# Kernel tuning notes

Measured on AMD Instinct MI355X. Metric: run time of the kernel, lower is better.

Reference implementation:

```python
import jax, jax.numpy as jnp
import numpy as np

EPS = 1e-8
SOFTEN = 1.0
COLOR_NORM = 1.0


def setup_inputs() -> dict:
    key = jax.random.key(0)
    k1, k2, k3, k4 = jax.random.split(key, 4)
    B, C, H, W = 16, 3, 224, 224
    K, HID = 64, 256
    img = jax.random.uniform(k1, (B, C, H, W), dtype=jnp.float32)
    W1 = jax.random.normal(k2, (HID, C), dtype=jnp.float32) * 0.1
    b1 = jax.random.normal(k3, (HID,), dtype=jnp.float32) * 0.1
    W2 = jax.random.normal(k4, (K, HID), dtype=jnp.float32) * 0.1
    return {"img": img, "W1": W1, "b1": b1, "W2": W2}


def reference(img, W1, b1, W2):
    # color_mask: 1x1 conv (3->256) + ReLU + 1x1 conv (256->K, no bias)
    h = jax.nn.relu(jnp.einsum('bchw,oc->bohw', img, W1) + b1[None, :, None, None])
    logits = jnp.einsum('bohw,ko->bkhw', h, W2)
    # Softmax2d == softmax over channel dim; soften=1
    m = jax.nn.softmax(SOFTEN * logits, axis=1)  # (B,K,H,W)
    # training=True path: soft weighted palette.
    # (img[:,:,None]*m[:,None]).sum(spatial) contracted directly via einsum
    # to avoid materializing the (B,3,K,H,W) broadcast tensor.
    num = jnp.einsum('bchw,bkhw->bck', img, m)          # (B,3,K)
    den = jnp.sum(m, axis=(2, 3))                        # (B,K)
    palette = num / (den[:, None, :] + EPS) / COLOR_NORM  # (B,3,K)
    # color_jitter=0 -> jitter_palette == palette
    transformed_img = jnp.einsum('bkhw,bck->bchw', m, palette)
    # match torch shape (B,3,K,1,1) for palette output
    return transformed_img, m, palette[:, :, :, None, None]
```

## Files before the change

kernel.cpp:

```cpp
#include <hip/hip_runtime.h>
#include <hip/hip_bf16.h>

#define BATCH 16
#define HW 50176
#define HID 256
#define K 64

#define OUT_T_OFF 0
#define OUT_M_OFF 2408448
#define OUT_P_OFF 53788672

#define WS_DEN 0
#define WS_NUM 1024
#define WS_W1P 4096
#define WS_W2B 5120

typedef short bf16x8 __attribute__((ext_vector_type(8)));
typedef float f32x4  __attribute__((ext_vector_type(4)));

static __device__ __forceinline__ short f2bf(float x) {
    union { __hip_bfloat16 h; short s; } u;
    u.h = __float2bfloat16(x);
    return u.s;
}

__global__ __launch_bounds__(256) void colorcnn_prep(
    const float* __restrict__ W1, const float* __restrict__ b1,
    const float* __restrict__ W2, float* __restrict__ wsf,
    float4* __restrict__ w1p, ushort* __restrict__ w2b)
{
    const int t = threadIdx.x;
    if (blockIdx.x == 0) {
#pragma unroll
        for (int q = 0; q < 16; ++q) wsf[q * 256 + t] = 0.f;
        w1p[t] = make_float4(W1[3 * t], W1[3 * t + 1], W1[3 * t + 2], b1[t]);
    }
#pragma unroll
    for (int q = 0; q < 8; ++q) {
        const int i = (blockIdx.x * 8 + q) * 256 + t;
        w2b[i] = (ushort)f2bf(W2[i]);
    }
}

__global__ __launch_bounds__(256) void colorcnn_mlp_softmax(
    const float* __restrict__ img, const float4* __restrict__ w1p,
    const ushort* __restrict__ w2b, float* __restrict__ m_out,
    float* __restrict__ den_ws, float* __restrict__ num_ws)
{
    __shared__ int4 lds[2304];
    __shared__ float sred[4][256];

    const int t = threadIdx.x;
    const int4* w2b16 = (const int4*)w2b;
#pragma unroll
    for (int q = 0; q < 8; ++q) {
        const int i = t + q * 256;
        const int n = i >> 5, s = i & 31;
        lds[n * 32 + (s ^ (n & 7))] = w2b16[i];
    }
    lds[2048 + (t ^ ((t >> 3) & 3))] = ((const int4*)w1p)[t];
    __syncthreads();

    const int b    = blockIdx.y;
    const int pb   = blockIdx.x * 256;
    const int w    = t >> 6;
    const int lane = t & 63;
    const int l15  = lane & 15;
    const int lg   = lane >> 4;
    const int pwb  = pb + w * 64;

    const float* ip = img + (size_t)b * 3 * HW;

    float rr[4], gg[4], uu[4];
#pragma unroll
    for (int s = 0; s < 4; ++s) {
        const int px = pwb + s * 16 + l15;
        rr[s] = ip[px]; gg[s] = ip[HW + px]; uu[s] = ip[2 * HW + px];
    }

    f32x4 acc[4][4];
#pragma unroll
    for (int s = 0; s < 4; ++s)
#pragma unroll
        for (int ni = 0; ni < 4; ++ni)
            acc[s][ni] = (f32x4){0.f, 0.f, 0.f, 0.f};

#pragma unroll
    for (int c = 0; c < 8; ++c) {
        bf16x8 a0, a1, a2, a3;
#pragma unroll
        for (int j = 0; j < 8; ++j) {
            const int hid = c * 32 + lg * 8 + j;
            const float4 wv = *(const float4*)&lds[2048 + (hid ^ lg)];
            float t0 = fmaf(rr[0], wv.x, fmaf(gg[0], wv.y, fmaf(uu[0], wv.z, wv.w)));
            float t1 = fmaf(rr[1], wv.x, fmaf(gg[1], wv.y, fmaf(uu[1], wv.z, wv.w)));
            float t2 = fmaf(rr[2], wv.x, fmaf(gg[2], wv.y, fmaf(uu[2], wv.z, wv.w)));
            float t3 = fmaf(rr[3], wv.x, fmaf(gg[3], wv.y, fmaf(uu[3], wv.z, wv.w)));
            a0[j] = f2bf(fmaxf(t0, 0.f));
            a1[j] = f2bf(fmaxf(t1, 0.f));
            a2[j] = f2bf(fmaxf(t2, 0.f));
            a3[j] = f2bf(fmaxf(t3, 0.f));
        }
#pragma unroll
        for (int ni = 0; ni < 4; ++ni) {
            const int n = ni * 16 + l15;
            const bf16x8 bf = *(const bf16x8*)&lds[n * 32 + (((c * 4 + lg) ^ (n & 7)))];
            acc[0][ni] = __builtin_amdgcn_mfma_f32_16x16x32_bf16(a0, bf, acc[0][ni], 0, 0, 0);
            acc[1][ni] = __builtin_amdgcn_mfma_f32_16x16x32_bf16(a1, bf, acc[1][ni], 0, 0, 0);
            acc[2][ni] = __builtin_amdgcn_mfma_f32_16x16x32_bf16(a2, bf, acc[2][ni], 0, 0, 0);
            acc[3][ni] = __builtin_amdgcn_mfma_f32_16x16x32_bf16(a3, bf, acc[3][ni], 0, 0, 0);
        }
    }

#pragma unroll
    for (int s = 0; s < 4; ++s) {
#pragma unroll
        for (int reg = 0; reg < 4; ++reg) {
            float v0 = __expf(acc[s][0][reg]);
            float v1 = __expf(acc[s][1][reg]);
            float v2 = __expf(acc[s][2][reg]);
            float v3 = __expf(acc[s][3][reg]);
            float sm = (v0 + v1) + (v2 + v3);
            sm += __shfl_xor(sm, 1);
            sm += __shfl_xor(sm, 2);
            sm += __shfl_xor(sm, 4);
            sm += __shfl_xor(sm, 8);
            const float inv = 1.f / sm;
            acc[s][0][reg] = v0 * inv; acc[s][1][reg] = v1 * inv;
            acc[s][2][reg] = v2 * inv; acc[s][3][reg] = v3 * inv;
        }
    }

    float red[16];
#pragma unroll
    for (int i = 0; i < 16; ++i) red[i] = 0.f;
#pragma unroll
    for (int s = 0; s < 4; ++s) {
        const int pxb = pwb + s * 16 + lg * 4;
        const f32x4 rC = *(const f32x4*)&ip[pxb];
        const f32x4 gC = *(const f32x4*)&ip[HW + pxb];
        const f32x4 uC = *(const f32x4*)&ip[2 * HW + pxb];
#pragma unroll
        for (int ni = 0; ni < 4; ++ni) {
#pragma unroll
            for (int reg = 0; reg < 4; ++reg) {
                const float mv = acc[s][ni][reg];
                red[ni]      += mv;
                red[4 + ni]   = fmaf(rC[reg], mv, red[4 + ni]);
                red[8 + ni]   = fmaf(gC[reg], mv, red[8 + ni]);
                red[12 + ni]  = fmaf(uC[reg], mv, red[12 + ni]);
            }
        }
    }
#pragma unroll
    for (int i = 0; i < 16; ++i) {
        red[i] += __shfl_xor(red[i], 16);
        red[i] += __shfl_xor(red[i], 32);
    }
    if (lg == 0) {
#pragma unroll
        for (int ni = 0; ni < 4; ++ni) {
            const int n = ni * 16 + l15;
            sred[w][n]       = red[ni];
            sred[w][64 + n]  = red[4 + ni];
            sred[w][128 + n] = red[8 + ni];
            sred[w][192 + n] = red[12 + ni];
        }
    }
    __syncthreads();
    {
        const int q = t >> 6, n = t & 63;
        const float v = sred[0][t] + sred[1][t] + sred[2][t] + sred[3][t];
        if (q == 0) atomicAdd(&den_ws[b * K + n], v);
        else        atomicAdd(&num_ws[(b * 3 + (q - 1)) * K + n], v);
    }

    float* mo = m_out + (size_t)b * K * HW + pwb;
#pragma unroll
    for (int s = 0; s < 4; ++s)
#pragma unroll
        for (int ni = 0; ni < 4; ++ni) {
            const int n = ni * 16 + l15;
            *(f32x4*)&mo[(size_t)n * HW + s * 16 + lg * 4] = acc[s][ni];
        }
}

__global__ __launch_bounds__(256) void colorcnn_reconstruct(
    const float* __restrict__ m, const float* __restrict__ den_ws,
    const float* __restrict__ num_ws, float* __restrict__ pal_out,
    float* __restrict__ t_out)
{
    __shared__ float pl[192];
    const int b    = blockIdx.x / 49;
    const int tile = blockIdx.x % 49;
    const int t    = threadIdx.x;

    if (t < 192) {
        const int c = t >> 6, k = t & 63;
        const float v = num_ws[(b * 3 + c) * K + k] / (den_ws[b * K + k] + 1e-8f);
        pl[t] = v;
        if (tile == 0) pal_out[b * 3 * K + t] = v;
    }
    __syncthreads();

    const int p = tile * 1024 + t * 4;
    const float* mp = m + (size_t)b * K * HW + p;
    f32x4 ar = {0.f, 0.f, 0.f, 0.f}, ag = ar, ab = ar;
#pragma unroll
    for (int k = 0; k < K; ++k) {
        const f32x4 mv = *(const f32x4*)&mp[(size_t)k * HW];
        const float pr = pl[k], pg = pl[K + k], pu = pl[2 * K + k];
#pragma unroll
        for (int j = 0; j < 4; ++j) {
            ar[j] = fmaf(mv[j], pr, ar[j]);
            ag[j] = fmaf(mv[j], pg, ag[j]);
            ab[j] = fmaf(mv[j], pu, ab[j]);
        }
    }
    float* to = t_out + (size_t)b * 3 * HW + p;
    *(f32x4*)&to[0]      = ar;
    *(f32x4*)&to[HW]     = ag;
    *(f32x4*)&to[2 * HW] = ab;
}

extern "C" void kernel_launch(void* const* d_in, const int* in_sizes, int n_in,
                              void* d_out, int out_size, void* d_ws, size_t ws_size,
                              hipStream_t stream) {
    const float* img = (const float*)d_in[0];
    const float* W1  = (const float*)d_in[1];
    const float* b1  = (const float*)d_in[2];
    const float* W2  = (const float*)d_in[3];

    float* out   = (float*)d_out;
    float* t_out = out + OUT_T_OFF;
    float* m_out = out + OUT_M_OFF;
    float* p_out = out + OUT_P_OFF;

    float*  wsf    = (float*)d_ws;
    float*  den_ws = wsf + WS_DEN;
    float*  num_ws = wsf + WS_NUM;
    float4* w1p    = (float4*)(wsf + WS_W1P);
    ushort* w2b    = (ushort*)(wsf + WS_W2B);

    colorcnn_prep<<<8, 256, 0, stream>>>(W1, b1, W2, wsf, w1p, w2b);
    colorcnn_mlp_softmax<<<dim3(HW / 256, BATCH), 256, 0, stream>>>(img, w1p, w2b, m_out, den_ws, num_ws);
    colorcnn_reconstruct<<<BATCH * 49, 256, 0, stream>>>(m_out, den_ws, num_ws, p_out, t_out);
}
```

Baseline: 125.0 us.

## Recompute MLP softmax in reconstruct kernel instead of rereading mask from memory

The reconstruct kernel no longer loads the large softmax mask from global memory. It restages the weights and recomputes the 1x1-conv MLP and softmax from the image, then applies the palette with in-register reductions and cross-lane shuffles. This removes a full read of the mask tensor in exchange for repeating the matrix-core work and weight staging. The mask stores in the first kernel also become nontemporal to reduce cache pollution.

```diff
diff --git a/kernel.cpp b/kernel.cpp
--- a/kernel.cpp
+++ b/kernel.cpp
@@ -42,6 +42,77 @@
     }
 }
 
+#define STAGE_WEIGHTS()                                                          \
+    {                                                                            \
+        const int4* w2b16 = (const int4*)w2b;                                    \
+        _Pragma("unroll")                                                        \
+        for (int q = 0; q < 8; ++q) {                                            \
+            const int i = threadIdx.x + q * 256;                                 \
+            const int n_ = i >> 5, s_ = i & 31;                                  \
+            lds[n_ * 32 + (s_ ^ (n_ & 7))] = w2b16[i];                           \
+        }                                                                        \
+        lds[2048 + (threadIdx.x ^ ((threadIdx.x >> 3) & 3))] =                   \
+            ((const int4*)w1p)[threadIdx.x];                                     \
+    }
+
+#define MLP_SOFTMAX_CORE()                                                       \
+    float rr[4], gg[4], uu[4];                                                   \
+    _Pragma("unroll")                                                            \
+    for (int s = 0; s < 4; ++s) {                                                \
+        const int px = pwb + s * 16 + l15;                                       \
+        rr[s] = ip[px]; gg[s] = ip[HW + px]; uu[s] = ip[2 * HW + px];            \
+    }                                                                            \
+    f32x4 acc[4][4];                                                             \
+    _Pragma("unroll")                                                            \
+    for (int s = 0; s < 4; ++s)                                                  \
+        _Pragma("unroll")                                                        \
+        for (int ni = 0; ni < 4; ++ni)                                           \
+            acc[s][ni] = (f32x4){0.f, 0.f, 0.f, 0.f};                            \
+    _Pragma("unroll")                                                            \
+    for (int c = 0; c < 8; ++c) {                                                \
+        bf16x8 a0, a1, a2, a3;                                                   \
+        _Pragma("unroll")                                                        \
+        for (int j = 0; j < 8; ++j) {                                            \
+            const int hid = c * 32 + lg * 8 + j;                                 \
+            const float4 wv = *(const float4*)&lds[2048 + (hid ^ lg)];           \
+            float t0 = fmaf(rr[0], wv.x, fmaf(gg[0], wv.y, fmaf(uu[0], wv.z, wv.w))); \
+            float t1 = fmaf(rr[1], wv.x, fmaf(gg[1], wv.y, fmaf(uu[1], wv.z, wv.w))); \
+            float t2 = fmaf(rr[2], wv.x, fmaf(gg[2], wv.y, fmaf(uu[2], wv.z, wv.w))); \
+            float t3 = fmaf(rr[3], wv.x, fmaf(gg[3], wv.y, fmaf(uu[3], wv.z, wv.w))); \
+            a0[j] = f2bf(fmaxf(t0, 0.f));                                        \
+            a1[j] = f2bf(fmaxf(t1, 0.f));                                        \
+            a2[j] = f2bf(fmaxf(t2, 0.f));                                        \
+            a3[j] = f2bf(fmaxf(t3, 0.f));                                        \
+        }                                                                        \
+        _Pragma("unroll")                                                        \
+        for (int ni = 0; ni < 4; ++ni) {                                         \
+            const int n = ni * 16 + l15;                                         \
+            const bf16x8 bf = *(const bf16x8*)&lds[n * 32 + (((c * 4 + lg) ^ (n & 7)))]; \
+            acc[0][ni] = __builtin_amdgcn_mfma_f32_16x16x32_bf16(a0, bf, acc[0][ni], 0, 0, 0); \
+            acc[1][ni] = __builtin_amdgcn_mfma_f32_16x16x32_bf16(a1, bf, acc[1][ni], 0, 0, 0); \
+            acc[2][ni] = __builtin_amdgcn_mfma_f32_16x16x32_bf16(a2, bf, acc[2][ni], 0, 0, 0); \
+            acc[3][ni] = __builtin_amdgcn_mfma_f32_16x16x32_bf16(a3, bf, acc[3][ni], 0, 0, 0); \
+        }                                                                        \
+    }                                                                            \
+    _Pragma("unroll")                                                            \
+    for (int s = 0; s < 4; ++s) {                                                \
+        _Pragma("unroll")                                                        \
+        for (int reg = 0; reg < 4; ++reg) {                                      \
+            float v0 = __expf(acc[s][0][reg]);                                   \
+            float v1 = __expf(acc[s][1][reg]);                                   \
+            float v2 = __expf(acc[s][2][reg]);                                   \
+            float v3 = __expf(acc[s][3][reg]);                                   \
+            float sm = (v0 + v1) + (v2 + v3);                                    \
+            sm += __shfl_xor(sm, 1);                                             \
+            sm += __shfl_xor(sm, 2);                                             \
+            sm += __shfl_xor(sm, 4);                                             \
+            sm += __shfl_xor(sm, 8);                                             \
+            const float inv = 1.f / sm;                                          \
+            acc[s][0][reg] = v0 * inv; acc[s][1][reg] = v1 * inv;                \
+            acc[s][2][reg] = v2 * inv; acc[s][3][reg] = v3 * inv;                \
+        }                                                                        \
+    }
+
 __global__ __launch_bounds__(256) void colorcnn_mlp_softmax(
     const float* __restrict__ img, const float4* __restrict__ w1p,
     const ushort* __restrict__ w2b, float* __restrict__ m_out,
@@ -50,86 +121,20 @@
     __shared__ int4 lds[2304];
     __shared__ float sred[4][256];
 
-    const int t = threadIdx.x;
-    const int4* w2b16 = (const int4*)w2b;
-#pragma unroll
-    for (int q = 0; q < 8; ++q) {
-        const int i = t + q * 256;
-        const int n = i >> 5, s = i & 31;
-        lds[n * 32 + (s ^ (n & 7))] = w2b16[i];
-    }
-    lds[2048 + (t ^ ((t >> 3) & 3))] = ((const int4*)w1p)[t];
+    STAGE_WEIGHTS();
     __syncthreads();
 
     const int b    = blockIdx.y;
     const int pb   = blockIdx.x * 256;
+    const int t    = threadIdx.x;
     const int w    = t >> 6;
     const int lane = t & 63;
     const int l15  = lane & 15;
     const int lg   = lane >> 4;
     const int pwb  = pb + w * 64;
-
     const float* ip = img + (size_t)b * 3 * HW;
 
-    float rr[4], gg[4], uu[4];
-#pragma unroll
-    for (int s = 0; s < 4; ++s) {
-        const int px = pwb + s * 16 + l15;
-        rr[s] = ip[px]; gg[s] = ip[HW + px]; uu[s] = ip[2 * HW + px];
-    }
-
-    f32x4 acc[4][4];
-#pragma unroll
-    for (int s = 0; s < 4; ++s)
-#pragma unroll
-        for (int ni = 0; ni < 4; ++ni)
-            acc[s][ni] = (f32x4){0.f, 0.f, 0.f, 0.f};
-
-#pragma unroll
-    for (int c = 0; c < 8; ++c) {
-        bf16x8 a0, a1, a2, a3;
-#pragma unroll
-        for (int j = 0; j < 8; ++j) {
-            const int hid = c * 32 + lg * 8 + j;
-            const float4 wv = *(const float4*)&lds[2048 + (hid ^ lg)];
-            float t0 = fmaf(rr[0], wv.x, fmaf(gg[0], wv.y, fmaf(uu[0], wv.z, wv.w)));
-            float t1 = fmaf(rr[1], wv.x, fmaf(gg[1], wv.y, fmaf(uu[1], wv.z, wv.w)));
-            float t2 = fmaf(rr[2], wv.x, fmaf(gg[2], wv.y, fmaf(uu[2], wv.z, wv.w)));
-            float t3 = fmaf(rr[3], wv.x, fmaf(gg[3], wv.y, fmaf(uu[3], wv.z, wv.w)));
-            a0[j] = f2bf(fmaxf(t0, 0.f));
-            a1[j] = f2bf(fmaxf(t1, 0.f));
-            a2[j] = f2bf(fmaxf(t2, 0.f));
-            a3[j] = f2bf(fmaxf(t3, 0.f));
-        }
-#pragma unroll
-        for (int ni = 0; ni < 4; ++ni) {
-            const int n = ni * 16 + l15;
-            const bf16x8 bf = *(const bf16x8*)&lds[n * 32 + (((c * 4 + lg) ^ (n & 7)))];
-            acc[0][ni] = __builtin_amdgcn_mfma_f32_16x16x32_bf16(a0, bf, acc[0][ni], 0, 0, 0);
-            acc[1][ni] = __builtin_amdgcn_mfma_f32_16x16x32_bf16(a1, bf, acc[1][ni], 0, 0, 0);
-            acc[2][ni] = __builtin_amdgcn_mfma_f32_16x16x32_bf16(a2, bf, acc[2][ni], 0, 0, 0);
-            acc[3][ni] = __builtin_amdgcn_mfma_f32_16x16x32_bf16(a3, bf, acc[3][ni], 0, 0, 0);
-        }
-    }
-
-#pragma unroll
-    for (int s = 0; s < 4; ++s) {
-#pragma unroll
-        for (int reg = 0; reg < 4; ++reg) {
-            float v0 = __expf(acc[s][0][reg]);
-            float v1 = __expf(acc[s][1][reg]);
-            float v2 = __expf(acc[s][2][reg]);
-            float v3 = __expf(acc[s][3][reg]);
-            float sm = (v0 + v1) + (v2 + v3);
-            sm += __shfl_xor(sm, 1);
-            sm += __shfl_xor(sm, 2);
-            sm += __shfl_xor(sm, 4);
-            sm += __shfl_xor(sm, 8);
-            const float inv = 1.f / sm;
-            acc[s][0][reg] = v0 * inv; acc[s][1][reg] = v1 * inv;
-            acc[s][2][reg] = v2 * inv; acc[s][3][reg] = v3 * inv;
-        }
-    }
+    MLP_SOFTMAX_CORE();
 
     float red[16];
 #pragma unroll
@@ -181,46 +186,81 @@
 #pragma unroll
         for (int ni = 0; ni < 4; ++ni) {
             const int n = ni * 16 + l15;
-            *(f32x4*)&mo[(size_t)n * HW + s * 16 + lg * 4] = acc[s][ni];
+            __builtin_nontemporal_store(acc[s][ni],
+                (f32x4*)&mo[(size_t)n * HW + s * 16 + lg * 4]);
         }
 }
 
 __global__ __launch_bounds__(256) void colorcnn_reconstruct(
-    const float* __restrict__ m, const float* __restrict__ den_ws,
+    const float* __restrict__ img, const float4* __restrict__ w1p,
+    const ushort* __restrict__ w2b, const float* __restrict__ den_ws,
     const float* __restrict__ num_ws, float* __restrict__ pal_out,
     float* __restrict__ t_out)
 {
+    __shared__ int4 lds[2304];
     __shared__ float pl[192];
-    const int b    = blockIdx.x / 49;
-    const int tile = blockIdx.x % 49;
+
+    STAGE_WEIGHTS();
+
+    const int b    = blockIdx.y;
+    const int pb   = blockIdx.x * 256;
     const int t    = threadIdx.x;
+    const int w    = t >> 6;
+    const int lane = t & 63;
+    const int l15  = lane & 15;
+    const int lg   = lane >> 4;
+    const int pwb  = pb + w * 64;
+    const float* ip = img + (size_t)b * 3 * HW;
 
     if (t < 192) {
         const int c = t >> 6, k = t & 63;
         const float v = num_ws[(b * 3 + c) * K + k] / (den_ws[b * K + k] + 1e-8f);
         pl[t] = v;
-        if (tile == 0) pal_out[b * 3 * K + t] = v;
+        if (blockIdx.x == 0) pal_out[b * 3 * K + t] = v;
     }
     __syncthreads();
 
-    const int p = tile * 1024 + t * 4;
-    const float* mp = m + (size_t)b * K * HW + p;
-    f32x4 ar = {0.f, 0.f, 0.f, 0.f}, ag = ar, ab = ar;
-#pragma unroll
-    for (int k = 0; k < K; ++k) {
-        const f32x4 mv = *(const f32x4*)&mp[(size_t)k * HW];
-        const float pr = pl[k], pg = pl[K + k], pu = pl[2 * K + k];
-#pragma unroll
-        for (int j = 0; j < 4; ++j) {
-            ar[j] = fmaf(mv[j], pr, ar[j]);
-            ag[j] = fmaf(mv[j], pg, ag[j]);
-            ab[j] = fmaf(mv[j], pu, ab[j]);
-        }
-    }
-    float* to = t_out + (size_t)b * 3 * HW + p;
-    *(f32x4*)&to[0]      = ar;
-    *(f32x4*)&to[HW]     = ag;
-    *(f32x4*)&to[2 * HW] = ab;
+    MLP_SOFTMAX_CORE();
+
+    float pc[3][4];
+#pragma unroll
+    for (int c = 0; c < 3; ++c)
+#pragma unroll
+        for (int ni = 0; ni < 4; ++ni)
+            pc[c][ni] = pl[c * K + ni * 16 + l15];
+
+    float* to = t_out + (size_t)b * 3 * HW;
+#pragma unroll
+    for (int s = 0; s < 4; ++s) {
+        float part[3][4];
+#pragma unroll
+        for (int c = 0; c < 3; ++c)
+#pragma unroll
+            for (int reg = 0; reg < 4; ++reg) {
+                float v = acc[s][0][reg] * pc[c][0];
+                v = fmaf(acc[s][1][reg], pc[c][1], v);
+                v = fmaf(acc[s][2][reg], pc[c][2], v);
+                v = fmaf(acc[s][3][reg], pc[c][3], v);
+                part[c][reg] = v;
+            }
+#pragma unroll
+        for (int c = 0; c < 3; ++c)
+#pragma unroll
+            for (int reg = 0; reg < 4; ++reg) {
+                part[c][reg] += __shfl_xor(part[c][reg], 1);
+                part[c][reg] += __shfl_xor(part[c][reg], 2);
+                part[c][reg] += __shfl_xor(part[c][reg], 4);
+                part[c][reg] += __shfl_xor(part[c][reg], 8);
+            }
+        if (l15 == 0) {
+            const int px = pwb + s * 16 + lg * 4;
+#pragma unroll
+            for (int c = 0; c < 3; ++c) {
+                f32x4 v = { part[c][0], part[c][1], part[c][2], part[c][3] };
+                *(f32x4*)&to[(size_t)c * HW + px] = v;
+            }
+        }
+    }
 }
 
 extern "C" void kernel_launch(void* const* d_in, const int* in_sizes, int n_in,
@@ -244,5 +284,5 @@
 
     colorcnn_prep<<<8, 256, 0, stream>>>(W1, b1, W2, wsf, w1p, w2b);
     colorcnn_mlp_softmax<<<dim3(HW / 256, BATCH), 256, 0, stream>>>(img, w1p, w2b, m_out, den_ws, num_ws);
-    colorcnn_reconstruct<<<BATCH * 49, 256, 0, stream>>>(m_out, den_ws, num_ws, p_out, t_out);
-}
+    colorcnn_reconstruct<<<dim3(HW / 256, BATCH), 256, 0, stream>>>(img, w1p, w2b, den_ws, num_ws, p_out, t_out);
+}
```

Result: slower. 164.5 us (+31.6%).

## Halve pixels per block in MLP kernel to raise occupancy, pack bf16 pairs

Applied to the files above, without the earlier changes.

Each wave now handles 32 pixels instead of 64, so the grid doubles and accumulator registers halve, with launch bounds asking for 4 blocks per SIMD group. The W1 LDS swizzle is removed in favour of a simple per-lane-group base pointer. Hidden activations are converted two at a time with the packed bf16 conversion, and the softmax reciprocal uses the hardware rcp. The aim is more waves in flight to hide memory latency, at the cost of reloading W2 into LDS for twice as many blocks and issuing twice as many atomics.

```diff
diff --git a/kernel.cpp b/kernel.cpp
--- a/kernel.cpp
+++ b/kernel.cpp
@@ -42,7 +42,7 @@
     }
 }
 
-__global__ __launch_bounds__(256) void colorcnn_mlp_softmax(
+__global__ __launch_bounds__(256, 4) void colorcnn_mlp_softmax(
     const float* __restrict__ img, const float4* __restrict__ w1p,
     const ushort* __restrict__ w2b, float* __restrict__ m_out,
     float* __restrict__ den_ws, float* __restrict__ num_ws)
@@ -58,74 +58,75 @@
         const int n = i >> 5, s = i & 31;
         lds[n * 32 + (s ^ (n & 7))] = w2b16[i];
     }
-    lds[2048 + (t ^ ((t >> 3) & 3))] = ((const int4*)w1p)[t];
+    lds[2048 + t] = ((const int4*)w1p)[t];
     __syncthreads();
 
     const int b    = blockIdx.y;
-    const int pb   = blockIdx.x * 256;
+    const int pb   = blockIdx.x * 128;
     const int w    = t >> 6;
     const int lane = t & 63;
     const int l15  = lane & 15;
     const int lg   = lane >> 4;
-    const int pwb  = pb + w * 64;
+    const int pwb  = pb + w * 32;
+    const int x7   = l15 & 7;
 
     const float* ip = img + (size_t)b * 3 * HW;
 
-    float rr[4], gg[4], uu[4];
-#pragma unroll
-    for (int s = 0; s < 4; ++s) {
+    float rr[2], gg[2], uu[2];
+#pragma unroll
+    for (int s = 0; s < 2; ++s) {
         const int px = pwb + s * 16 + l15;
         rr[s] = ip[px]; gg[s] = ip[HW + px]; uu[s] = ip[2 * HW + px];
     }
 
-    f32x4 acc[4][4];
-#pragma unroll
-    for (int s = 0; s < 4; ++s)
+    f32x4 acc[2][4];
+#pragma unroll
+    for (int s = 0; s < 2; ++s)
 #pragma unroll
         for (int ni = 0; ni < 4; ++ni)
             acc[s][ni] = (f32x4){0.f, 0.f, 0.f, 0.f};
 
+    const float4* w1l = (const float4*)&lds[2048 + lg * 8];
+
 #pragma unroll
     for (int c = 0; c < 8; ++c) {
-        bf16x8 a0, a1, a2, a3;
-#pragma unroll
-        for (int j = 0; j < 8; ++j) {
-            const int hid = c * 32 + lg * 8 + j;
-            const float4 wv = *(const float4*)&lds[2048 + (hid ^ lg)];
-            float t0 = fmaf(rr[0], wv.x, fmaf(gg[0], wv.y, fmaf(uu[0], wv.z, wv.w)));
-            float t1 = fmaf(rr[1], wv.x, fmaf(gg[1], wv.y, fmaf(uu[1], wv.z, wv.w)));
-            float t2 = fmaf(rr[2], wv.x, fmaf(gg[2], wv.y, fmaf(uu[2], wv.z, wv.w)));
-            float t3 = fmaf(rr[3], wv.x, fmaf(gg[3], wv.y, fmaf(uu[3], wv.z, wv.w)));
-            a0[j] = f2bf(fmaxf(t0, 0.f));
-            a1[j] = f2bf(fmaxf(t1, 0.f));
-            a2[j] = f2bf(fmaxf(t2, 0.f));
-            a3[j] = f2bf(fmaxf(t3, 0.f));
-        }
-#pragma unroll
-        for (int ni = 0; ni < 4; ++ni) {
-            const int n = ni * 16 + l15;
-            const bf16x8 bf = *(const bf16x8*)&lds[n * 32 + (((c * 4 + lg) ^ (n & 7)))];
-            acc[0][ni] = __builtin_amdgcn_mfma_f32_16x16x32_bf16(a0, bf, acc[0][ni], 0, 0, 0);
-            acc[1][ni] = __builtin_amdgcn_mfma_f32_16x16x32_bf16(a1, bf, acc[1][ni], 0, 0, 0);
-            acc[2][ni] = __builtin_amdgcn_mfma_f32_16x16x32_bf16(a2, bf, acc[2][ni], 0, 0, 0);
-            acc[3][ni] = __builtin_amdgcn_mfma_f32_16x16x32_bf16(a3, bf, acc[3][ni], 0, 0, 0);
-        }
-    }
-
-#pragma unroll
-    for (int s = 0; s < 4; ++s) {
+        union { bf16x8 v; unsigned int u[4]; } ua0, ua1;
+#pragma unroll
+        for (int p = 0; p < 4; ++p) {
+            const float4 wv0 = w1l[c * 32 + 2 * p];
+            const float4 wv1 = w1l[c * 32 + 2 * p + 1];
+            const float e0 = fmaxf(fmaf(rr[0], wv0.x, fmaf(gg[0], wv0.y, fmaf(uu[0], wv0.z, wv0.w))), 0.f);
+            const float o0 = fmaxf(fmaf(rr[0], wv1.x, fmaf(gg[0], wv1.y, fmaf(uu[0], wv1.z, wv1.w))), 0.f);
+            const float e1 = fmaxf(fmaf(rr[1], wv0.x, fmaf(gg[1], wv0.y, fmaf(uu[1], wv0.z, wv0.w))), 0.f);
+            const float o1 = fmaxf(fmaf(rr[1], wv1.x, fmaf(gg[1], wv1.y, fmaf(uu[1], wv1.z, wv1.w))), 0.f);
+            __hip_bfloat162 c0 = __float22bfloat162_rn(float2{e0, o0});
+            __hip_bfloat162 c1 = __float22bfloat162_rn(float2{e1, o1});
+            ua0.u[p] = *(unsigned int*)&c0;
+            ua1.u[p] = *(unsigned int*)&c1;
+        }
+        const int sw = (c * 4 + lg) ^ x7;
+#pragma unroll
+        for (int ni = 0; ni < 4; ++ni) {
+            const bf16x8 bf = *(const bf16x8*)&lds[(ni * 16 + l15) * 32 + sw];
+            acc[0][ni] = __builtin_amdgcn_mfma_f32_16x16x32_bf16(ua0.v, bf, acc[0][ni], 0, 0, 0);
+            acc[1][ni] = __builtin_amdgcn_mfma_f32_16x16x32_bf16(ua1.v, bf, acc[1][ni], 0, 0, 0);
+        }
+    }
+
+#pragma unroll
+    for (int s = 0; s < 2; ++s) {
 #pragma unroll
         for (int reg = 0; reg < 4; ++reg) {
-            float v0 = __expf(acc[s][0][reg]);
-            float v1 = __expf(acc[s][1][reg]);
-            float v2 = __expf(acc[s][2][reg]);
-            float v3 = __expf(acc[s][3][reg]);
+            const float v0 = __expf(acc[s][0][reg]);
+            const float v1 = __expf(acc[s][1][reg]);
+            const float v2 = __expf(acc[s][2][reg]);
+            const float v3 = __expf(acc[s][3][reg]);
             float sm = (v0 + v1) + (v2 + v3);
             sm += __shfl_xor(sm, 1);
             sm += __shfl_xor(sm, 2);
             sm += __shfl_xor(sm, 4);
             sm += __shfl_xor(sm, 8);
-            const float inv = 1.f / sm;
+            const float inv = __builtin_amdgcn_rcpf(sm);
             acc[s][0][reg] = v0 * inv; acc[s][1][reg] = v1 * inv;
             acc[s][2][reg] = v2 * inv; acc[s][3][reg] = v3 * inv;
         }
@@ -135,7 +136,7 @@
 #pragma unroll
     for (int i = 0; i < 16; ++i) red[i] = 0.f;
 #pragma unroll
-    for (int s = 0; s < 4; ++s) {
+    for (int s = 0; s < 2; ++s) {
         const int pxb = pwb + s * 16 + lg * 4;
         const f32x4 rC = *(const f32x4*)&ip[pxb];
         const f32x4 gC = *(const f32x4*)&ip[HW + pxb];
@@ -177,7 +178,7 @@
 
     float* mo = m_out + (size_t)b * K * HW + pwb;
 #pragma unroll
-    for (int s = 0; s < 4; ++s)
+    for (int s = 0; s < 2; ++s)
 #pragma unroll
         for (int ni = 0; ni < 4; ++ni) {
             const int n = ni * 16 + l15;
@@ -243,6 +244,6 @@
     ushort* w2b    = (ushort*)(wsf + WS_W2B);
 
     colorcnn_prep<<<8, 256, 0, stream>>>(W1, b1, W2, wsf, w1p, w2b);
-    colorcnn_mlp_softmax<<<dim3(HW / 256, BATCH), 256, 0, stream>>>(img, w1p, w2b, m_out, den_ws, num_ws);
+    colorcnn_mlp_softmax<<<dim3(HW / 128, BATCH), 256, 0, stream>>>(img, w1p, w2b, m_out, den_ws, num_ws);
     colorcnn_reconstruct<<<BATCH * 49, 256, 0, stream>>>(m_out, den_ws, num_ws, p_out, t_out);
 }
```

Result: no change. 125.0 us (-0.0%).
